# Performance work log

Hardware: AMD Instinct MI355X
Metric: run time of the kernel (lower is better)

Reference implementation:

```python
import jax, jax.numpy as jnp
import numpy as np

NA, NQ, FDIM, NC, HID = 512, 4096, 2, 16, 64
CUTOFF = 6.0
GAMMA = 10.0
BOX = 12.0


def setup_inputs() -> dict:
    key = jax.random.key(0)
    ks = jax.random.split(key, 16)
    s = lambda k, shp, fan: jax.random.normal(k, shp, jnp.float32) * (1.0 / np.sqrt(fan))
    return {
        "atom_pos": jax.random.uniform(ks[0], (NA, 3), jnp.float32) * BOX,
        "atom_feat": jax.random.normal(ks[1], (NA, FDIM), jnp.float32),
        "query_pos": jax.random.uniform(ks[2], (NQ, 3), jnp.float32) * BOX,
        "W1": s(ks[3], (FDIM + NC, HID), FDIM + NC), "b1": jnp.zeros((HID,), jnp.float32),
        "W2": s(ks[4], (HID, HID), HID), "b2": jnp.zeros((HID,), jnp.float32),
        "W3": s(ks[5], (HID, HID // 2), HID), "b3": jnp.zeros((HID // 2,), jnp.float32),
        "W4": s(ks[6], (HID // 2, 1), HID // 2), "b4": jnp.zeros((1,), jnp.float32),
        "W5": s(ks[7], (3, 64), 3), "b5": jnp.zeros((64,), jnp.float32),
        "W6": s(ks[8], (64, 3), 64), "b6": jnp.zeros((3,), jnp.float32),
    }


def _forward(atom_pos, atom_feat, query_pos, W1, b1, W2, b2, W3, b3, W4, b4, W5, b5, W6, b6):
    centers = jnp.linspace(0.0, CUTOFF, NC, dtype=jnp.float32)  # RBF centers
    rel = query_pos[:, None, :] - atom_pos[None, :, :]          # (Nq,Na,3)
    dist = jnp.linalg.norm(rel + 1e-12, axis=-1)                 # (Nq,Na) (matches torch.norm(rel+eps))
    mask = (dist <= CUTOFF).astype(dist.dtype)
    rbf = jnp.exp(-GAMMA * (dist[..., None] - centers) ** 2)     # (Nq,Na,Nc)
    feat_b = jnp.broadcast_to(atom_feat[None], (query_pos.shape[0],) + atom_feat.shape)
    atom_input = jnp.concatenate([feat_b, rbf], axis=-1)         # (Nq,Na,F+Nc)
    h = jax.nn.relu(atom_input @ W1 + b1)
    h = jax.nn.relu(h @ W2 + b2)                                 # (Nq,Na,H)
    scalar_w = (jax.nn.relu(h @ W3 + b3) @ W4 + b4)[..., 0] * mask  # (Nq,Na)
    dir_vec = rel / (dist[..., None] + 1e-12)                    # (Nq,Na,3)
    weighted = jnp.einsum('qa,qad->qd', scalar_w, dir_vec)       # (Nq,3)
    out = jax.nn.relu(weighted @ W5 + b5) @ W6 + b6              # (Nq,3)
    return out


def reference(atom_pos, atom_feat, query_pos, W1, b1, W2, b2, W3, b3, W4, b4, W5, b5, W6, b6):
    return _forward(atom_pos, atom_feat, query_pos, W1, b1, W2, b2, W3, b3, W4, b4, W5, b5, W6, b6)
```

## Files before the change

kernel.cpp:

```cpp
#include <hip/hip_runtime.h>
#include <math.h>


typedef _Float16 f16x4 __attribute__((ext_vector_type(4)));
typedef _Float16 f16x2 __attribute__((ext_vector_type(2)));
typedef float    f32x4 __attribute__((ext_vector_type(4)));

#define CAP 352
#define NT  2

#define MFMA16(A,B,C) __builtin_amdgcn_mfma_f32_16x16x16f16(A,B,C,0,0,0)

__device__ __forceinline__ float exp2_fast(float x) {
    float r;
    asm("v_exp_f32 %0, %1" : "=v"(r) : "v"(x));
    return r;
}

__device__ __forceinline__ f16x4 relu_cvt(f32x4 c) {
    return f16x4{(_Float16)fmaxf(c[0],0.f), (_Float16)fmaxf(c[1],0.f),
                 (_Float16)fmaxf(c[2],0.f), (_Float16)fmaxf(c[3],0.f)};
}

__device__ __forceinline__ float pack_f16x2(float a, float b) {
    f16x2 h{(_Float16)a, (_Float16)b};
    return __builtin_bit_cast(float, h);
}

__global__ __launch_bounds__(64) void repack_kernel(
    const float* __restrict__ W1, const float* __restrict__ b1,
    const float* __restrict__ W2, const float* __restrict__ b2,
    const float* __restrict__ W3, const float* __restrict__ b3,
    const float* __restrict__ W4, char* __restrict__ ws)
{
    const int b = blockIdx.x, l = threadIdx.x;
    const int col = l & 15, quad = l >> 4;
    if (b < 32) {
        f16x4 v;
        #pragma unroll
        for (int j = 0; j < 4; ++j) {
            float x;
            if (b < 8) {
                const int kc = b >> 2, mt = b & 3;
                const int k = kc*16 + quad*4 + j;
                if (k < 16)       x = W1[(k+2)*64 + mt*16 + col];
                else if (k == 16) x = W1[        mt*16 + col];
                else if (k == 17) x = W1[ 64   + mt*16 + col];
                else if (k == 18) x = b1[        mt*16 + col];
                else              x = 0.0f;
            } else if (b < 24) {
                const int idx = b - 8, kc = idx >> 2, mt = idx & 3;
                const int k = kc*16 + quad*4 + j;
                x = W2[k*64 + mt*16 + col];
            } else {
                const int idx = b - 24, kc = idx >> 1, mt = idx & 1;
                const int k = kc*16 + quad*4 + j;
                x = W3[k*32 + mt*16 + col];
            }
            v[j] = (_Float16)x;
        }
        *(f16x4*)(ws + (b*64 + l)*8) = v;
    } else {
        float* bo = (float*)(ws + 16384);
        #pragma unroll
        for (int i = l; i < 128; i += 64) {
            float x;
            if (i < 64)       x = b2[i];
            else if (i < 96)  x = b3[i - 64];
            else              x = W4[i - 96];
            bo[i] = x;
        }
    }
}

__global__ __launch_bounds__(256, 4) void aqfn_kernel(
    const float* __restrict__ atom_pos,
    const float* __restrict__ atom_feat,
    const float* __restrict__ query_pos,
    const float* __restrict__ b4,
    const float* __restrict__ W5, const float* __restrict__ b5,
    const float* __restrict__ W6, const float* __restrict__ b6,
    const char*  __restrict__ ws,
    float* __restrict__ out)
{
    __shared__ __align__(16) float4 rbufs[4][CAP];
    __shared__ __align__(16) f16x4  wlds[2048];
    __shared__ __align__(16) float  biaslds[128];

    const int tid  = threadIdx.x;
    const int wave = __builtin_amdgcn_readfirstlane(tid >> 6);
    const int lane = tid & 63;
    const int col  = lane & 15;
    const int quad = lane >> 4;
    const int q    = blockIdx.x * 4 + wave;

    float4* rb = rbufs[wave];

    {
        const f16x4* wsrc = (const f16x4*)ws;
        #pragma unroll
        for (int i = 0; i < 8; ++i)
            wlds[tid + i*256] = wsrc[tid + i*256];
        if (tid < 128) biaslds[tid] = ((const float*)(ws + 16384))[tid];
    }

    const float b4v = b4[0];

    const float qx = query_pos[q*3+0];
    const float qy = query_pos[q*3+1];
    const float qz = query_pos[q*3+2];

    int off = 0;
    #pragma unroll
    for (int it = 0; it < 8; ++it) {
        const int a = it*64 + lane;
        const float rx = qx - atom_pos[a*3+0];
        const float ry = qy - atom_pos[a*3+1];
        const float rz = qz - atom_pos[a*3+2];
        const float f0 = atom_feat[a*2+0];
        const float f1 = atom_feat[a*2+1];
        const float ex = __fadd_rn(rx, 1e-12f);
        const float ey = __fadd_rn(ry, 1e-12f);
        const float ez = __fadd_rn(rz, 1e-12f);
        const float dd = __fadd_rn(__fadd_rn(__fmul_rn(ex,ex), __fmul_rn(ey,ey)),
                                   __fmul_rn(ez,ez));
        const float dist = sqrtf(dd);
        const unsigned long long m = __ballot(dist <= 6.0f);
        const int p = off + (int)__popcll(m & ((1ull << lane) - 1ull));
        if (((m >> lane) & 1ull) && p < CAP)
            rb[p] = make_float4(rx, ry, rz, pack_f16x2(f0, f1));
        off += (int)__popcll(m);
    }
    const int count = off > CAP ? CAP : off;

    __syncthreads();

    float wacc0 = 0.f, wacc1 = 0.f, wacc2 = 0.f;
    const int nchunks = (count + (NT*16 - 1)) / (NT*16);
    const float cbase = 1.5193132f * (float)(quad*4);

    #pragma unroll 1
    for (int chunk = 0; chunk < nchunks; ++chunk) {
        const int row0 = chunk * (NT*16);

        int wb = 0;
        asm volatile("" : "+v"(wb));
        const float4* bias4 = (const float4*)biaslds;

        float4 rv[NT]; float dvv[NT]; f16x2 ffv[NT];
        #pragma unroll
        for (int u = 0; u < NT; ++u) {
            int pr = row0 + u*16 + col;
            if (pr >= count) pr = count - 1;
            rv[u] = rb[pr];
        }
        #pragma unroll
        for (int u = 0; u < NT; ++u) {
            ffv[u] = __builtin_bit_cast(f16x2, rv[u].w);
            const float ex = __fadd_rn(rv[u].x, 1e-12f);
            const float ey = __fadd_rn(rv[u].y, 1e-12f);
            const float ez = __fadd_rn(rv[u].z, 1e-12f);
            const float dd = __fadd_rn(__fadd_rn(__fmul_rn(ex,ex), __fmul_rn(ey,ey)),
                                       __fmul_rn(ez,ez));
            dvv[u] = sqrtf(dd);
        }

        f16x4 xa0[NT], xa1[NT];
        #pragma unroll
        for (int u = 0; u < NT; ++u) {
            const float base = __fmul_rn(dvv[u], 3.7982831f) - cbase;
            #pragma unroll
            for (int j = 0; j < 4; ++j) {
                const float t = base - 1.5193132f * (float)j;
                xa0[u][j] = (_Float16)exp2_fast(t * -t);
            }
            const bool q0 = (quad == 0);
            xa1[u] = f16x4{q0 ? ffv[u][0] : (_Float16)0.f,
                           q0 ? ffv[u][1] : (_Float16)0.f,
                           (_Float16)(q0 ? 1.f : 0.f),
                           (_Float16)0.f};
        }

        f16x4 t1[2][4];
        #pragma unroll
        for (int kc = 0; kc < 2; ++kc)
            #pragma unroll
            for (int mt = 0; mt < 4; ++mt)
                t1[kc][mt] = wlds[wb + (kc*4 + mt)*64 + lane];
        f16x4 a2[NT][4];
        #pragma unroll
        for (int u = 0; u < NT; ++u)
            #pragma unroll
            for (int mt = 0; mt < 4; ++mt) {
                f32x4 c = {0.f, 0.f, 0.f, 0.f};
                c = MFMA16(t1[0][mt], xa0[u], c);
                c = MFMA16(t1[1][mt], xa1[u], c);
                a2[u][mt] = relu_cvt(c);
            }

        f16x4 t2[4][4];
        #pragma unroll
        for (int kc = 0; kc < 4; ++kc)
            #pragma unroll
            for (int mt = 0; mt < 4; ++mt)
                t2[kc][mt] = wlds[wb + (8 + kc*4 + mt)*64 + lane];
        float4 b2v[4];
        #pragma unroll
        for (int mt = 0; mt < 4; ++mt) b2v[mt] = bias4[wb + mt*4 + quad];
        f16x4 a3[NT][4];
        #pragma unroll
        for (int u = 0; u < NT; ++u)
            #pragma unroll
            for (int mt = 0; mt < 4; ++mt) {
                f32x4 c = {b2v[mt].x, b2v[mt].y, b2v[mt].z, b2v[mt].w};
                #pragma unroll
                for (int kc = 0; kc < 4; ++kc)
                    c = MFMA16(t2[kc][mt], a2[u][kc], c);
                a3[u][mt] = relu_cvt(c);
            }

        f16x4 t3[4][2];
        #pragma unroll
        for (int kc = 0; kc < 4; ++kc)
            #pragma unroll
            for (int mt = 0; mt < 2; ++mt)
                t3[kc][mt] = wlds[wb + (24 + kc*2 + mt)*64 + lane];
        float4 b3v[2], w4v[2];
        #pragma unroll
        for (int mt = 0; mt < 2; ++mt) {
            b3v[mt] = bias4[wb + 16 + mt*4 + quad];
            w4v[mt] = bias4[wb + 24 + mt*4 + quad];
        }
        #pragma unroll
        for (int u = 0; u < NT; ++u) {
            float s = 0.f;
            #pragma unroll
            for (int mt = 0; mt < 2; ++mt) {
                f32x4 c = {b3v[mt].x, b3v[mt].y, b3v[mt].z, b3v[mt].w};
                #pragma unroll
                for (int kc = 0; kc < 4; ++kc)
                    c = MFMA16(t3[kc][mt], a3[u][kc], c);
                const float* wv = &w4v[mt].x;
                #pragma unroll
                for (int rr = 0; rr < 4; ++rr)
                    s = fmaf(fmaxf(c[rr], 0.f), wv[rr], s);
            }
            s += __shfl_xor(s, 16);
            s += __shfl_xor(s, 32);
            s += b4v;
            const int   p2  = row0 + u*16 + col;
            const float inv = __builtin_amdgcn_rcpf(dvv[u] + 1e-12f);
            const float wm  = (p2 < count) ? (s * inv) : 0.f;
            wacc0 = fmaf(wm, rv[u].x, wacc0);
            wacc1 = fmaf(wm, rv[u].y, wacc1);
            wacc2 = fmaf(wm, rv[u].z, wacc2);
        }
    }

    #pragma unroll
    for (int o = 1; o < 64; o <<= 1) {
        wacc0 += __shfl_xor(wacc0, o);
        wacc1 += __shfl_xor(wacc1, o);
        wacc2 += __shfl_xor(wacc2, o);
    }
    const float v0 = wacc0 * 0.25f;
    const float v1 = wacc1 * 0.25f;
    const float v2 = wacc2 * 0.25f;

    int hz = 0;
    asm volatile("" : "+v"(hz));
    const float w5x = W5[hz + lane];
    const float w5y = W5[hz + 64 + lane];
    const float w5z = W5[hz + 128 + lane];
    const float b5v = b5[hz + lane];
    float th = fmaf(v0, w5x, fmaf(v1, w5y, fmaf(v2, w5z, b5v)));
    th = fmaxf(th, 0.f);
    float o0 = th * W6[hz + lane*3+0];
    float o1 = th * W6[hz + lane*3+1];
    float o2 = th * W6[hz + lane*3+2];
    #pragma unroll
    for (int o = 1; o < 64; o <<= 1) {
        o0 += __shfl_xor(o0, o);
        o1 += __shfl_xor(o1, o);
        o2 += __shfl_xor(o2, o);
    }
    if (lane == 0) {
        out[q*3+0] = o0 + b6[0];
        out[q*3+1] = o1 + b6[1];
        out[q*3+2] = o2 + b6[2];
    }
}

extern "C" void kernel_launch(void* const* d_in, const int* in_sizes, int n_in,
                              void* d_out, int out_size, void* d_ws, size_t ws_size,
                              hipStream_t stream) {
    const float* atom_pos  = (const float*)d_in[0];
    const float* atom_feat = (const float*)d_in[1];
    const float* query_pos = (const float*)d_in[2];
    const float* W1 = (const float*)d_in[3];  const float* b1 = (const float*)d_in[4];
    const float* W2 = (const float*)d_in[5];  const float* b2 = (const float*)d_in[6];
    const float* W3 = (const float*)d_in[7];  const float* b3 = (const float*)d_in[8];
    const float* W4 = (const float*)d_in[9];  const float* b4 = (const float*)d_in[10];
    const float* W5 = (const float*)d_in[11]; const float* b5 = (const float*)d_in[12];
    const float* W6 = (const float*)d_in[13]; const float* b6 = (const float*)d_in[14];
    float* out = (float*)d_out;
    char*  ws  = (char*)d_ws;

    hipLaunchKernelGGL(repack_kernel, dim3(33), dim3(64), 0, stream,
                       W1, b1, W2, b2, W3, b3, W4, ws);
    hipLaunchKernelGGL(aqfn_kernel, dim3(1024), dim3(256), 0, stream,
                       atom_pos, atom_feat, query_pos, b4, W5, b5, W6, b6,
                       (const char*)ws, out);
}
```

Baseline: 112.3 us.

## Precompute per-atom MLP table over distance and interpolate per query

```diff
diff --git a/kernel.cpp b/kernel.cpp
--- a/kernel.cpp
+++ b/kernel.cpp
@@ -6,8 +6,8 @@
 typedef _Float16 f16x2 __attribute__((ext_vector_type(2)));
 typedef float    f32x4 __attribute__((ext_vector_type(4)));
 
-#define CAP 352
-#define NT  2
+#define NT 2
+#define NS 512
 
 #define MFMA16(A,B,C) __builtin_amdgcn_mfma_f32_16x16x16f16(A,B,C,0,0,0)
 
@@ -20,11 +20,6 @@
 __device__ __forceinline__ f16x4 relu_cvt(f32x4 c) {
     return f16x4{(_Float16)fmaxf(c[0],0.f), (_Float16)fmaxf(c[1],0.f),
                  (_Float16)fmaxf(c[2],0.f), (_Float16)fmaxf(c[3],0.f)};
-}
-
-__device__ __forceinline__ float pack_f16x2(float a, float b) {
-    f16x2 h{(_Float16)a, (_Float16)b};
-    return __builtin_bit_cast(float, h);
 }
 
 __global__ __launch_bounds__(64) void repack_kernel(
@@ -73,28 +68,20 @@
     }
 }
 
-__global__ __launch_bounds__(256, 4) void aqfn_kernel(
-    const float* __restrict__ atom_pos,
+__global__ __launch_bounds__(256, 4) void tabgen_kernel(
     const float* __restrict__ atom_feat,
-    const float* __restrict__ query_pos,
     const float* __restrict__ b4,
-    const float* __restrict__ W5, const float* __restrict__ b5,
-    const float* __restrict__ W6, const float* __restrict__ b6,
     const char*  __restrict__ ws,
-    float* __restrict__ out)
+    float* __restrict__ tab)
 {
-    __shared__ __align__(16) float4 rbufs[4][CAP];
-    __shared__ __align__(16) f16x4  wlds[2048];
-    __shared__ __align__(16) float  biaslds[128];
+    __shared__ __align__(16) f16x4 wlds[2048];
+    __shared__ __align__(16) float biaslds[128];
 
     const int tid  = threadIdx.x;
     const int wave = __builtin_amdgcn_readfirstlane(tid >> 6);
     const int lane = tid & 63;
     const int col  = lane & 15;
     const int quad = lane >> 4;
-    const int q    = blockIdx.x * 4 + wave;
-
-    float4* rb = rbufs[wave];
 
     {
         const f16x4* wsrc = (const f16x4*)ws;
@@ -103,169 +90,170 @@
             wlds[tid + i*256] = wsrc[tid + i*256];
         if (tid < 128) biaslds[tid] = ((const float*)(ws + 16384))[tid];
     }
-
+    __syncthreads();
+
+    const int c  = blockIdx.x * 4 + wave;
+    const int a  = c >> 4;
+    const int i0 = (c & 15) * 32;
+    const float f0 = atom_feat[a*2+0];
+    const float f1 = atom_feat[a*2+1];
     const float b4v = b4[0];
+    const float4* bias4 = (const float4*)biaslds;
+
+    const float cbase = 1.5193132f * (float)(quad*4);
+
+    f16x4 xa0[NT], xa1[NT];
+    #pragma unroll
+    for (int u = 0; u < NT; ++u) {
+        const int   idx  = i0 + u*16 + col;
+        const float dist = (float)idx * (6.0f/511.0f);
+        const float base = __fmul_rn(dist, 3.7982831f) - cbase;
+        #pragma unroll
+        for (int j = 0; j < 4; ++j) {
+            const float t = base - 1.5193132f * (float)j;
+            xa0[u][j] = (_Float16)exp2_fast(t * -t);
+        }
+        const bool q0 = (quad == 0);
+        xa1[u] = f16x4{q0 ? (_Float16)f0 : (_Float16)0.f,
+                       q0 ? (_Float16)f1 : (_Float16)0.f,
+                       (_Float16)(q0 ? 1.f : 0.f),
+                       (_Float16)0.f};
+    }
+
+    f16x4 t1[2][4];
+    #pragma unroll
+    for (int kc = 0; kc < 2; ++kc)
+        #pragma unroll
+        for (int mt = 0; mt < 4; ++mt)
+            t1[kc][mt] = wlds[(kc*4 + mt)*64 + lane];
+    f16x4 a2[NT][4];
+    #pragma unroll
+    for (int u = 0; u < NT; ++u)
+        #pragma unroll
+        for (int mt = 0; mt < 4; ++mt) {
+            f32x4 cc = {0.f, 0.f, 0.f, 0.f};
+            cc = MFMA16(t1[0][mt], xa0[u], cc);
+            cc = MFMA16(t1[1][mt], xa1[u], cc);
+            a2[u][mt] = relu_cvt(cc);
+        }
+
+    f16x4 t2[4][4];
+    #pragma unroll
+    for (int kc = 0; kc < 4; ++kc)
+        #pragma unroll
+        for (int mt = 0; mt < 4; ++mt)
+            t2[kc][mt] = wlds[(8 + kc*4 + mt)*64 + lane];
+    float4 b2v[4];
+    #pragma unroll
+    for (int mt = 0; mt < 4; ++mt) b2v[mt] = bias4[mt*4 + quad];
+    f16x4 a3[NT][4];
+    #pragma unroll
+    for (int u = 0; u < NT; ++u)
+        #pragma unroll
+        for (int mt = 0; mt < 4; ++mt) {
+            f32x4 cc = {b2v[mt].x, b2v[mt].y, b2v[mt].z, b2v[mt].w};
+            #pragma unroll
+            for (int kc = 0; kc < 4; ++kc)
+                cc = MFMA16(t2[kc][mt], a2[u][kc], cc);
+            a3[u][mt] = relu_cvt(cc);
+        }
+
+    f16x4 t3[4][2];
+    #pragma unroll
+    for (int kc = 0; kc < 4; ++kc)
+        #pragma unroll
+        for (int mt = 0; mt < 2; ++mt)
+            t3[kc][mt] = wlds[(24 + kc*2 + mt)*64 + lane];
+    float4 b3v[2], w4v[2];
+    #pragma unroll
+    for (int mt = 0; mt < 2; ++mt) {
+        b3v[mt] = bias4[16 + mt*4 + quad];
+        w4v[mt] = bias4[24 + mt*4 + quad];
+    }
+    #pragma unroll
+    for (int u = 0; u < NT; ++u) {
+        float s = 0.f;
+        #pragma unroll
+        for (int mt = 0; mt < 2; ++mt) {
+            f32x4 cc = {b3v[mt].x, b3v[mt].y, b3v[mt].z, b3v[mt].w};
+            #pragma unroll
+            for (int kc = 0; kc < 4; ++kc)
+                cc = MFMA16(t3[kc][mt], a3[u][kc], cc);
+            const float* wv = &w4v[mt].x;
+            #pragma unroll
+            for (int rr = 0; rr < 4; ++rr)
+                s = fmaf(fmaxf(cc[rr], 0.f), wv[rr], s);
+        }
+        s += __shfl_xor(s, 16);
+        s += __shfl_xor(s, 32);
+        s += b4v;
+        if (quad == 0)
+            tab[a*NS + i0 + u*16 + col] = s;
+    }
+}
+
+__global__ __launch_bounds__(256, 4) void field_kernel(
+    const float* __restrict__ atom_pos,
+    const float* __restrict__ query_pos,
+    const float* __restrict__ W5, const float* __restrict__ b5,
+    const float* __restrict__ W6, const float* __restrict__ b6,
+    const float* __restrict__ tab,
+    float* __restrict__ out)
+{
+    __shared__ float px[512], py[512], pz[512];
+
+    const int tid  = threadIdx.x;
+    const int wave = __builtin_amdgcn_readfirstlane(tid >> 6);
+    const int lane = tid & 63;
+    const int q    = blockIdx.x * 4 + wave;
+
+    #pragma unroll
+    for (int i = tid; i < 512; i += 256) {
+        px[i] = atom_pos[i*3+0];
+        py[i] = atom_pos[i*3+1];
+        pz[i] = atom_pos[i*3+2];
+    }
+    __syncthreads();
 
     const float qx = query_pos[q*3+0];
     const float qy = query_pos[q*3+1];
     const float qz = query_pos[q*3+2];
 
-    int off = 0;
+    float acc0 = 0.f, acc1 = 0.f, acc2 = 0.f;
     #pragma unroll
     for (int it = 0; it < 8; ++it) {
         const int a = it*64 + lane;
-        const float rx = qx - atom_pos[a*3+0];
-        const float ry = qy - atom_pos[a*3+1];
-        const float rz = qz - atom_pos[a*3+2];
-        const float f0 = atom_feat[a*2+0];
-        const float f1 = atom_feat[a*2+1];
+        const float rx = qx - px[a];
+        const float ry = qy - py[a];
+        const float rz = qz - pz[a];
         const float ex = __fadd_rn(rx, 1e-12f);
         const float ey = __fadd_rn(ry, 1e-12f);
         const float ez = __fadd_rn(rz, 1e-12f);
         const float dd = __fadd_rn(__fadd_rn(__fmul_rn(ex,ex), __fmul_rn(ey,ey)),
                                    __fmul_rn(ez,ez));
         const float dist = sqrtf(dd);
-        const unsigned long long m = __ballot(dist <= 6.0f);
-        const int p = off + (int)__popcll(m & ((1ull << lane) - 1ull));
-        if (((m >> lane) & 1ull) && p < CAP)
-            rb[p] = make_float4(rx, ry, rz, pack_f16x2(f0, f1));
-        off += (int)__popcll(m);
-    }
-    const int count = off > CAP ? CAP : off;
-
-    __syncthreads();
-
-    float wacc0 = 0.f, wacc1 = 0.f, wacc2 = 0.f;
-    const int nchunks = (count + (NT*16 - 1)) / (NT*16);
-    const float cbase = 1.5193132f * (float)(quad*4);
-
-    #pragma unroll 1
-    for (int chunk = 0; chunk < nchunks; ++chunk) {
-        const int row0 = chunk * (NT*16);
-
-        int wb = 0;
-        asm volatile("" : "+v"(wb));
-        const float4* bias4 = (const float4*)biaslds;
-
-        float4 rv[NT]; float dvv[NT]; f16x2 ffv[NT];
-        #pragma unroll
-        for (int u = 0; u < NT; ++u) {
-            int pr = row0 + u*16 + col;
-            if (pr >= count) pr = count - 1;
-            rv[u] = rb[pr];
-        }
-        #pragma unroll
-        for (int u = 0; u < NT; ++u) {
-            ffv[u] = __builtin_bit_cast(f16x2, rv[u].w);
-            const float ex = __fadd_rn(rv[u].x, 1e-12f);
-            const float ey = __fadd_rn(rv[u].y, 1e-12f);
-            const float ez = __fadd_rn(rv[u].z, 1e-12f);
-            const float dd = __fadd_rn(__fadd_rn(__fmul_rn(ex,ex), __fmul_rn(ey,ey)),
-                                       __fmul_rn(ez,ez));
-            dvv[u] = sqrtf(dd);
-        }
-
-        f16x4 xa0[NT], xa1[NT];
-        #pragma unroll
-        for (int u = 0; u < NT; ++u) {
-            const float base = __fmul_rn(dvv[u], 3.7982831f) - cbase;
-            #pragma unroll
-            for (int j = 0; j < 4; ++j) {
-                const float t = base - 1.5193132f * (float)j;
-                xa0[u][j] = (_Float16)exp2_fast(t * -t);
-            }
-            const bool q0 = (quad == 0);
-            xa1[u] = f16x4{q0 ? ffv[u][0] : (_Float16)0.f,
-                           q0 ? ffv[u][1] : (_Float16)0.f,
-                           (_Float16)(q0 ? 1.f : 0.f),
-                           (_Float16)0.f};
-        }
-
-        f16x4 t1[2][4];
-        #pragma unroll
-        for (int kc = 0; kc < 2; ++kc)
-            #pragma unroll
-            for (int mt = 0; mt < 4; ++mt)
-                t1[kc][mt] = wlds[wb + (kc*4 + mt)*64 + lane];
-        f16x4 a2[NT][4];
-        #pragma unroll
-        for (int u = 0; u < NT; ++u)
-            #pragma unroll
-            for (int mt = 0; mt < 4; ++mt) {
-                f32x4 c = {0.f, 0.f, 0.f, 0.f};
-                c = MFMA16(t1[0][mt], xa0[u], c);
-                c = MFMA16(t1[1][mt], xa1[u], c);
-                a2[u][mt] = relu_cvt(c);
-            }
-
-        f16x4 t2[4][4];
-        #pragma unroll
-        for (int kc = 0; kc < 4; ++kc)
-            #pragma unroll
-            for (int mt = 0; mt < 4; ++mt)
-                t2[kc][mt] = wlds[wb + (8 + kc*4 + mt)*64 + lane];
-        float4 b2v[4];
-        #pragma unroll
-        for (int mt = 0; mt < 4; ++mt) b2v[mt] = bias4[wb + mt*4 + quad];
-        f16x4 a3[NT][4];
-        #pragma unroll
-        for (int u = 0; u < NT; ++u)
-            #pragma unroll
-            for (int mt = 0; mt < 4; ++mt) {
-                f32x4 c = {b2v[mt].x, b2v[mt].y, b2v[mt].z, b2v[mt].w};
-                #pragma unroll
-                for (int kc = 0; kc < 4; ++kc)
-                    c = MFMA16(t2[kc][mt], a2[u][kc], c);
-                a3[u][mt] = relu_cvt(c);
-            }
-
-        f16x4 t3[4][2];
-        #pragma unroll
-        for (int kc = 0; kc < 4; ++kc)
-            #pragma unroll
-            for (int mt = 0; mt < 2; ++mt)
-                t3[kc][mt] = wlds[wb + (24 + kc*2 + mt)*64 + lane];
-        float4 b3v[2], w4v[2];
-        #pragma unroll
-        for (int mt = 0; mt < 2; ++mt) {
-            b3v[mt] = bias4[wb + 16 + mt*4 + quad];
-            w4v[mt] = bias4[wb + 24 + mt*4 + quad];
-        }
-        #pragma unroll
-        for (int u = 0; u < NT; ++u) {
-            float s = 0.f;
-            #pragma unroll
-            for (int mt = 0; mt < 2; ++mt) {
-                f32x4 c = {b3v[mt].x, b3v[mt].y, b3v[mt].z, b3v[mt].w};
-                #pragma unroll
-                for (int kc = 0; kc < 4; ++kc)
-                    c = MFMA16(t3[kc][mt], a3[u][kc], c);
-                const float* wv = &w4v[mt].x;
-                #pragma unroll
-                for (int rr = 0; rr < 4; ++rr)
-                    s = fmaf(fmaxf(c[rr], 0.f), wv[rr], s);
-            }
-            s += __shfl_xor(s, 16);
-            s += __shfl_xor(s, 32);
-            s += b4v;
-            const int   p2  = row0 + u*16 + col;
-            const float inv = __builtin_amdgcn_rcpf(dvv[u] + 1e-12f);
-            const float wm  = (p2 < count) ? (s * inv) : 0.f;
-            wacc0 = fmaf(wm, rv[u].x, wacc0);
-            wacc1 = fmaf(wm, rv[u].y, wacc1);
-            wacc2 = fmaf(wm, rv[u].z, wacc2);
-        }
+        const bool  in   = dist <= 6.0f;
+        const float t  = __fmul_rn(dist, 85.166664f);
+        int   i  = (int)t;
+        i = i < (NS-2) ? i : (NS-2);
+        const float frac = t - (float)i;
+        const float* row = tab + a*NS;
+        const float s0 = row[i];
+        const float s1 = row[i+1];
+        const float sv = fmaf(frac, s1 - s0, s0);
+        const float inv = __builtin_amdgcn_rcpf(dist + 1e-12f);
+        const float wm  = in ? sv * inv : 0.f;
+        acc0 = fmaf(wm, rx, acc0);
+        acc1 = fmaf(wm, ry, acc1);
+        acc2 = fmaf(wm, rz, acc2);
     }
 
     #pragma unroll
     for (int o = 1; o < 64; o <<= 1) {
-        wacc0 += __shfl_xor(wacc0, o);
-        wacc1 += __shfl_xor(wacc1, o);
-        wacc2 += __shfl_xor(wacc2, o);
-    }
-    const float v0 = wacc0 * 0.25f;
-    const float v1 = wacc1 * 0.25f;
-    const float v2 = wacc2 * 0.25f;
+        acc0 += __shfl_xor(acc0, o);
+        acc1 += __shfl_xor(acc1, o);
+        acc2 += __shfl_xor(acc2, o);
+    }
 
     int hz = 0;
     asm volatile("" : "+v"(hz));
@@ -273,7 +261,7 @@
     const float w5y = W5[hz + 64 + lane];
     const float w5z = W5[hz + 128 + lane];
     const float b5v = b5[hz + lane];
-    float th = fmaf(v0, w5x, fmaf(v1, w5y, fmaf(v2, w5z, b5v)));
+    float th = fmaf(acc0, w5x, fmaf(acc1, w5y, fmaf(acc2, w5z, b5v)));
     th = fmaxf(th, 0.f);
     float o0 = th * W6[hz + lane*3+0];
     float o1 = th * W6[hz + lane*3+1];
@@ -305,10 +293,13 @@
     const float* W6 = (const float*)d_in[13]; const float* b6 = (const float*)d_in[14];
     float* out = (float*)d_out;
     char*  ws  = (char*)d_ws;
+    float* tab = (float*)(ws + 32768);
 
     hipLaunchKernelGGL(repack_kernel, dim3(33), dim3(64), 0, stream,
                        W1, b1, W2, b2, W3, b3, W4, ws);
-    hipLaunchKernelGGL(aqfn_kernel, dim3(1024), dim3(256), 0, stream,
-                       atom_pos, atom_feat, query_pos, b4, W5, b5, W6, b6,
-                       (const char*)ws, out);
-}
+    hipLaunchKernelGGL(tabgen_kernel, dim3(2048), dim3(256), 0, stream,
+                       atom_feat, b4, (const char*)ws, tab);
+    hipLaunchKernelGGL(field_kernel, dim3(1024), dim3(256), 0, stream,
+                       atom_pos, query_pos, W5, b5, W6, b6,
+                       (const float*)tab, out);
+}
```

Result: faster. 100.9 us (-10.2%).
